# Optimization experiments

Measured on AMD Instinct MI355X. Metric: run time of the kernel, lower is better.

Reference implementation:

```python
import jax, jax.numpy as jnp
import numpy as np

KH, KW = 3, 3
DIL = 1
PH = DIL * (KH - 1) // 2
PW = DIL * (KW - 1) // 2


def setup_inputs() -> dict:
    key = jax.random.key(0)
    kq, kk = jax.random.split(key)
    B, C, H, W = 8, 128, 128, 128
    Q = jax.random.normal(kq, (B, C, H, W), dtype=jnp.float32)
    K = jax.random.normal(kk, (B, C, H, W), dtype=jnp.float32)
    return {"Q": Q, "K": K}


def reference(Q, K):
    # output[b, i*KW+j, h, w] = sum_c Q[b,c,h,w] * K_padded[b,c,h+i*DIL, w+j*DIL]
    B, C, H, W = Q.shape
    Kp = jnp.pad(K, ((0, 0), (0, 0), (PH, PH), (PW, PW)))
    outs = []
    for i in range(KH):
        for j in range(KW):
            Ks = Kp[:, :, i * DIL:i * DIL + H, j * DIL:j * DIL + W]  # shifted K window
            outs.append(jnp.sum(Q * Ks, axis=1))  # reduce over channels -> (B,H,W)
    return jnp.stack(outs, axis=1)  # (B, KH*KW, H, W)
```

## Files before the change

### kernel.cpp

```cpp
#include <hip/hip_runtime.h>


#define Bn 8
#define Cn 128
#define Hn 128
#define Wn 128
#define HWn (Hn * Wn)
#define CSPLIT 4
#define CCHUNK (Cn / CSPLIT)
#define OUTN (Bn * 9 * HWn)

template <bool ATOMIC>
__global__ __launch_bounds__(256) void msa_conv_part(
    const float* __restrict__ Q, const float* __restrict__ K,
    float* __restrict__ dst) {
  const int w  = threadIdx.x;
  const int h  = blockIdx.x * 2 + threadIdx.y;
  const int b  = blockIdx.y;
  const int cs = blockIdx.z;

  const bool wm  = (w > 0), wp  = (w < Wn - 1);
  const bool hmv = (h > 0), hpv = (h < Hn - 1);

  const int hm = hmv ? h - 1 : h + 1;
  const int hp = hpv ? h + 1 : h - 1;
  const int dm = wm ? -1 : +1;
  const int dp = wp ? +1 : -1;

  const size_t bk = (size_t)b * Cn * HWn + (size_t)cs * CCHUNK * HWn;
  const float* q  = Q + bk + (size_t)h * Wn + w;
  const float* km = K + bk + (size_t)hm * Wn + w;
  const float* k0 = K + bk + (size_t)h  * Wn + w;
  const float* kp = K + bk + (size_t)hp * Wn + w;
  const float* kmL = km + dm; const float* kmR = km + dp;
  const float* k0L = k0 + dm; const float* k0R = k0 + dp;
  const float* kpL = kp + dm; const float* kpR = kp + dp;

  float a00 = 0.f, a01 = 0.f, a02 = 0.f;
  float a10 = 0.f, a11 = 0.f, a12 = 0.f;
  float a20 = 0.f, a21 = 0.f, a22 = 0.f;

#pragma unroll 4
  for (int c = 0; c < CCHUNK; ++c) {
    const float qv = *q;
    const float m0 = *kmL, m1 = *km, m2 = *kmR;
    const float z0 = *k0L, z1 = *k0, z2 = *k0R;
    const float p0 = *kpL, p1 = *kp, p2 = *kpR;
    a00 += qv * m0; a01 += qv * m1; a02 += qv * m2;
    a10 += qv * z0; a11 += qv * z1; a12 += qv * z2;
    a20 += qv * p0; a21 += qv * p1; a22 += qv * p2;
    q += HWn;
    km += HWn; kmL += HWn; kmR += HWn;
    k0 += HWn; k0L += HWn; k0R += HWn;
    kp += HWn; kpL += HWn; kpR += HWn;
  }

  float res[9];
  res[0] = (hmv && wm) ? a00 : 0.f;
  res[1] = hmv ? a01 : 0.f;
  res[2] = (hmv && wp) ? a02 : 0.f;
  res[3] = wm ? a10 : 0.f;
  res[4] = a11;
  res[5] = wp ? a12 : 0.f;
  res[6] = (hpv && wm) ? a20 : 0.f;
  res[7] = hpv ? a21 : 0.f;
  res[8] = (hpv && wp) ? a22 : 0.f;

  const size_t o = (size_t)b * 9 * HWn + (size_t)h * Wn + w;
  if (ATOMIC) {
#pragma unroll
    for (int t = 0; t < 9; ++t)
      atomicAdd(dst + o + (size_t)t * HWn, res[t]);
  } else {
    float* p = dst + (size_t)cs * OUTN + o;
#pragma unroll
    for (int t = 0; t < 9; ++t) {
      *p = res[t];
      p += HWn;
    }
  }
}

__global__ __launch_bounds__(256) void msa_reduce4(
    const float* __restrict__ part, float* __restrict__ out) {
  const int i = blockIdx.x * 256 + threadIdx.x;
  const float4* p = (const float4*)part;
  const int n4 = OUTN / 4;
  float4 s0 = p[i];
  float4 s1 = p[n4 + i];
  float4 s2 = p[2 * n4 + i];
  float4 s3 = p[3 * n4 + i];
  float4 r;
  r.x = (s0.x + s1.x) + (s2.x + s3.x);
  r.y = (s0.y + s1.y) + (s2.y + s3.y);
  r.z = (s0.z + s1.z) + (s2.z + s3.z);
  r.w = (s0.w + s1.w) + (s2.w + s3.w);
  ((float4*)out)[i] = r;
}

__global__ __launch_bounds__(256) void msa_zero(float* __restrict__ out) {
  const int i = blockIdx.x * 256 + threadIdx.x;
  ((float4*)out)[i] = make_float4(0.f, 0.f, 0.f, 0.f);
}

extern "C" void kernel_launch(void* const* d_in, const int* in_sizes, int n_in,
                              void* d_out, int out_size, void* d_ws,
                              size_t ws_size, hipStream_t stream) {
  const float* Q = (const float*)d_in[0];
  const float* K = (const float*)d_in[1];
  float* out = (float*)d_out;

  dim3 block(128, 2);
  dim3 grid(Hn / 2, Bn, CSPLIT);

  const size_t ws_need = (size_t)CSPLIT * OUTN * sizeof(float);
  if (ws_size >= ws_need) {
    float* part = (float*)d_ws;
    msa_conv_part<false><<<grid, block, 0, stream>>>(Q, K, part);
    msa_reduce4<<<OUTN / 4 / 256, 256, 0, stream>>>(part, out);
  } else {
    msa_zero<<<OUTN / 4 / 256, 256, 0, stream>>>(out);
    msa_conv_part<true><<<grid, block, 0, stream>>>(Q, K, out);
  }
}
```

Baseline: 157.4 us.

## Vectorize conv to four columns per thread with wave shuffles for halo

Each thread now handles four adjacent columns using float4 loads of Q and three K rows, and gets the left and right neighbor values through wavefront shuffles. This replaces nine scalar K loads per channel with three vector loads, cutting load instructions and redundant cache traffic. The thread-to-row mapping changes so each 64-lane wavefront covers two rows of 32 lanes. The partial outputs are written as float4 stores. Each thread now keeps 36 accumulators, which raises register pressure, and there are fewer threads in total.

After: 154.7 us. No clear change (-1.7%).

```diff
diff --git a/kernel.cpp b/kernel.cpp
--- a/kernel.cpp
+++ b/kernel.cpp
@@ -11,72 +11,96 @@
 #define OUTN (Bn * 9 * HWn)
 
 template <bool ATOMIC>
-__global__ __launch_bounds__(256) void msa_conv_part(
+__global__ __launch_bounds__(256) void msa_conv_v4(
     const float* __restrict__ Q, const float* __restrict__ K,
     float* __restrict__ dst) {
-  const int w  = threadIdx.x;
-  const int h  = blockIdx.x * 2 + threadIdx.y;
-  const int b  = blockIdx.y;
-  const int cs = blockIdx.z;
+  const int tid  = threadIdx.x;
+  const int lane = tid & 63;
+  const int wq   = lane & 31;
+  const int rl   = lane >> 5;
+  const int wv   = tid >> 6;
+  const int h0   = blockIdx.x * 8;
+  const int r    = h0 + wv * 2 + rl;
+  const int b    = blockIdx.y;
+  const int cs   = blockIdx.z;
+  const int w0   = wq * 4;
 
-  const bool wm  = (w > 0), wp  = (w < Wn - 1);
-  const bool hmv = (h > 0), hpv = (h < Hn - 1);
+  const int rm = (r > 0) ? r - 1 : r + 1;
+  const int rp = (r < Hn - 1) ? r + 1 : r - 1;
 
-  const int hm = hmv ? h - 1 : h + 1;
-  const int hp = hpv ? h + 1 : h - 1;
-  const int dm = wm ? -1 : +1;
-  const int dp = wp ? +1 : -1;
+  const size_t base = (size_t)b * Cn * HWn + (size_t)cs * CCHUNK * HWn;
+  const float* qp = Q + base + (size_t)r  * Wn + w0;
+  const float* mp = K + base + (size_t)rm * Wn + w0;
+  const float* zp = K + base + (size_t)r  * Wn + w0;
+  const float* pp = K + base + (size_t)rp * Wn + w0;
 
-  const size_t bk = (size_t)b * Cn * HWn + (size_t)cs * CCHUNK * HWn;
-  const float* q  = Q + bk + (size_t)h * Wn + w;
-  const float* km = K + bk + (size_t)hm * Wn + w;
-  const float* k0 = K + bk + (size_t)h  * Wn + w;
-  const float* kp = K + bk + (size_t)hp * Wn + w;
-  const float* kmL = km + dm; const float* kmR = km + dp;
-  const float* k0L = k0 + dm; const float* k0R = k0 + dp;
-  const float* kpL = kp + dm; const float* kpR = kp + dp;
+  float acc[9][4];
+#pragma unroll
+  for (int t = 0; t < 9; ++t)
+#pragma unroll
+    for (int k = 0; k < 4; ++k) acc[t][k] = 0.f;
 
-  float a00 = 0.f, a01 = 0.f, a02 = 0.f;
-  float a10 = 0.f, a11 = 0.f, a12 = 0.f;
-  float a20 = 0.f, a21 = 0.f, a22 = 0.f;
+#define ACC4(t, s0, s1, s2, s3) \
+  acc[t][0] += q4.x * (s0);     \
+  acc[t][1] += q4.y * (s1);     \
+  acc[t][2] += q4.z * (s2);     \
+  acc[t][3] += q4.w * (s3);
 
-#pragma unroll 4
+#pragma unroll 2
   for (int c = 0; c < CCHUNK; ++c) {
-    const float qv = *q;
-    const float m0 = *kmL, m1 = *km, m2 = *kmR;
-    const float z0 = *k0L, z1 = *k0, z2 = *k0R;
-    const float p0 = *kpL, p1 = *kp, p2 = *kpR;
-    a00 += qv * m0; a01 += qv * m1; a02 += qv * m2;
-    a10 += qv * z0; a11 += qv * z1; a12 += qv * z2;
-    a20 += qv * p0; a21 += qv * p1; a22 += qv * p2;
-    q += HWn;
-    km += HWn; kmL += HWn; kmR += HWn;
-    k0 += HWn; k0L += HWn; k0R += HWn;
-    kp += HWn; kpL += HWn; kpR += HWn;
+    const float4 q4 = *(const float4*)qp;
+    const float4 m4 = *(const float4*)mp;
+    const float4 z4 = *(const float4*)zp;
+    const float4 p4 = *(const float4*)pp;
+    const float mL = __shfl_up(m4.w, 1, 64);
+    const float zL = __shfl_up(z4.w, 1, 64);
+    const float pL = __shfl_up(p4.w, 1, 64);
+    const float mR = __shfl_down(m4.x, 1, 64);
+    const float zR = __shfl_down(z4.x, 1, 64);
+    const float pR = __shfl_down(p4.x, 1, 64);
+
+    ACC4(0, mL,   m4.x, m4.y, m4.z)
+    ACC4(1, m4.x, m4.y, m4.z, m4.w)
+    ACC4(2, m4.y, m4.z, m4.w, mR)
+    ACC4(3, zL,   z4.x, z4.y, z4.z)
+    ACC4(4, z4.x, z4.y, z4.z, z4.w)
+    ACC4(5, z4.y, z4.z, z4.w, zR)
+    ACC4(6, pL,   p4.x, p4.y, p4.z)
+    ACC4(7, p4.x, p4.y, p4.z, p4.w)
+    ACC4(8, p4.y, p4.z, p4.w, pR)
+
+    qp += HWn; mp += HWn; zp += HWn; pp += HWn;
+  }
+#undef ACC4
+
+  if (wq == 0)  { acc[0][0] = 0.f; acc[3][0] = 0.f; acc[6][0] = 0.f; }
+  if (wq == 31) { acc[2][3] = 0.f; acc[5][3] = 0.f; acc[8][3] = 0.f; }
+  if (r == 0) {
+#pragma unroll
+    for (int t = 0; t < 3; ++t)
+#pragma unroll
+      for (int k = 0; k < 4; ++k) acc[t][k] = 0.f;
+  }
+  if (r == Hn - 1) {
+#pragma unroll
+    for (int t = 6; t < 9; ++t)
+#pragma unroll
+      for (int k = 0; k < 4; ++k) acc[t][k] = 0.f;
   }
 
-  float res[9];
-  res[0] = (hmv && wm) ? a00 : 0.f;
-  res[1] = hmv ? a01 : 0.f;
-  res[2] = (hmv && wp) ? a02 : 0.f;
-  res[3] = wm ? a10 : 0.f;
-  res[4] = a11;
-  res[5] = wp ? a12 : 0.f;
-  res[6] = (hpv && wm) ? a20 : 0.f;
-  res[7] = hpv ? a21 : 0.f;
-  res[8] = (hpv && wp) ? a22 : 0.f;
-
-  const size_t o = (size_t)b * 9 * HWn + (size_t)h * Wn + w;
+  const size_t o = (size_t)b * 9 * HWn + (size_t)r * Wn + w0;
   if (ATOMIC) {
 #pragma unroll
     for (int t = 0; t < 9; ++t)
-      atomicAdd(dst + o + (size_t)t * HWn, res[t]);
+#pragma unroll
+      for (int k = 0; k < 4; ++k)
+        atomicAdd(dst + o + (size_t)t * HWn + k, acc[t][k]);
   } else {
     float* p = dst + (size_t)cs * OUTN + o;
 #pragma unroll
     for (int t = 0; t < 9; ++t) {
-      *p = res[t];
-      p += HWn;
+      *(float4*)(p + (size_t)t * HWn) =
+          make_float4(acc[t][0], acc[t][1], acc[t][2], acc[t][3]);
     }
   }
 }
@@ -110,16 +134,16 @@
   const float* K = (const float*)d_in[1];
   float* out = (float*)d_out;
 
-  dim3 block(128, 2);
-  dim3 grid(Hn / 2, Bn, CSPLIT);
+  dim3 block(256);
+  dim3 grid(Hn / 8, Bn, CSPLIT);
 
   const size_t ws_need = (size_t)CSPLIT * OUTN * sizeof(float);
   if (ws_size >= ws_need) {
     float* part = (float*)d_ws;
-    msa_conv_part<false><<<grid, block, 0, stream>>>(Q, K, part);
+    msa_conv_v4<false><<<grid, block, 0, stream>>>(Q, K, part);
     msa_reduce4<<<OUTN / 4 / 256, 256, 0, stream>>>(part, out);
   } else {
     msa_zero<<<OUTN / 4 / 256, 256, 0, stream>>>(out);
-    msa_conv_part<true><<<grid, block, 0, stream>>>(Q, K, out);
+    msa_conv_v4<true><<<grid, block, 0, stream>>>(Q, K, out);
   }
 }
```
